# Performance work log

Hardware: AMD Instinct MI355X
Metric: run time of the kernel (lower is better)

## Reference

```python
import jax, jax.numpy as jnp
import numpy as np
import math

B, T, C = 2, 2048, 2048
N_HEAD = 16
N_KV = 4
GROUP = N_HEAD // N_KV
HS = C // N_HEAD
WINDOW = 1024
SINK = 4


def setup_inputs() -> dict:
    key = jax.random.key(0)
    ks = jax.random.split(key, 5)
    s = 1.0 / math.sqrt(C)
    return {
        "x": jax.random.normal(ks[0], (B, T, C), dtype=jnp.float32),
        "Wq": jax.random.normal(ks[1], (C, C), dtype=jnp.float32) * s,
        "Wk": jax.random.normal(ks[2], (N_KV * HS, C), dtype=jnp.float32) * s,
        "Wv": jax.random.normal(ks[3], (N_KV * HS, C), dtype=jnp.float32) * s,
        "Wo": jax.random.normal(ks[4], (C, C), dtype=jnp.float32) * s,
    }


def _sliding_window_sink_mask(t):
    i = jnp.arange(t)[:, None]  # query index
    j = jnp.arange(t)[None, :]  # key index
    causal = j <= i
    band = j >= i - (WINDOW - 1)
    mask = causal & band
    mask = mask | (j < SINK)          # sink columns always visible
    mask = mask & ((i >= SINK) | causal)  # sink rows stay strictly causal
    return mask  # (T, T) bool


def reference(x, Wq, Wk, Wv, Wo):
    b, t, c = x.shape
    q = (x @ Wq.T).reshape(b, t, N_HEAD, HS).transpose(0, 2, 1, 3)
    # group q heads by kv head: (B, n_kv, group, T, hs)
    q = q.reshape(b, N_KV, GROUP, t, HS)
    k = (x @ Wk.T).reshape(b, t, N_KV, HS).transpose(0, 2, 1, 3)  # (B, n_kv, T, hs)
    v = (x @ Wv.T).reshape(b, t, N_KV, HS).transpose(0, 2, 1, 3)
    scale = 1.0 / math.sqrt(HS)
    # scores over full TxT (faithful to original, K/V expansion done via broadcast)
    att = jnp.einsum('bkgqd,bkjd->bkgqj', q, k) * scale
    mask = _sliding_window_sink_mask(t)  # (T, T)
    att = jnp.where(mask[None, None, None, :, :], att, -jnp.inf)
    att = jax.nn.softmax(att, axis=-1)
    y = jnp.einsum('bkgqj,bkjd->bkgqd', att, v)
    y = y.reshape(b, N_HEAD, t, HS).transpose(0, 2, 1, 3).reshape(b, t, c)
    return y @ Wo.T
```

## Files before the change

### kernel.cpp

```cpp
#include <hip/hip_runtime.h>


#define T_SEQ 2048
#define NKV   4
#define HS    128
#define CDIM  2048
#define QKVN  3072
#define WIN   1024
#define SINKN 4
#define PSTR  68

typedef __bf16 bf16x8 __attribute__((ext_vector_type(8)));
typedef float  f32x4  __attribute__((ext_vector_type(4)));

#define MFMA16(A, B, C) __builtin_amdgcn_mfma_f32_16x16x32_bf16(A, B, C, 0, 0, 0)
#define EXP2(x) __builtin_amdgcn_exp2f(x)

__device__ inline unsigned short f2bu(float f) {
  unsigned int u = __float_as_uint(f);
  u += 0x7fffu + ((u >> 16) & 1u);
  return (unsigned short)(u >> 16);
}
__device__ inline unsigned int pkhi(float f0, float f1) {
  return __builtin_amdgcn_perm(__float_as_uint(f1), __float_as_uint(f0),
                               0x07060302u);
}
__device__ inline __bf16 us2b(unsigned short u) {
  union { unsigned short u; __bf16 b; } t; t.u = u; return t.b;
}
__device__ inline f32x4 fzero4() { f32x4 z = {0.f, 0.f, 0.f, 0.f}; return z; }

__device__ __forceinline__ void glds16(const void* g, const void* lds_uniform) {
  typedef __attribute__((address_space(1))) void gv;
  typedef __attribute__((address_space(3))) void lv;
  __builtin_amdgcn_global_load_lds((gv*)(unsigned long long)g,
                                   (lv*)(unsigned int)(unsigned long long)lds_uniform,
                                   16, 0, 0);
}

#define SZ_X  8388608
#define SZ_WQ 4194304
#define SZ_WK 1048576
#define OFF_WQ (SZ_X)
#define OFF_WK (SZ_X + SZ_WQ)
#define OFF_WV (OFF_WK + SZ_WK)
#define OFF_WO (OFF_WV + SZ_WK)
#define SZ_ALL (OFF_WO + SZ_WQ)

__global__ __launch_bounds__(256) void f2b_all(const float* __restrict__ x,
                                               const float* __restrict__ wq,
                                               const float* __restrict__ wk,
                                               const float* __restrict__ wv,
                                               const float* __restrict__ wo,
                                               unsigned short* __restrict__ out,
                                               float qs) {
  int i = (blockIdx.x * 256 + threadIdx.x) * 4;
  const float* src; int off; float sc = 1.0f;
  if (i < OFF_WQ)      { src = x;  off = 0; }
  else if (i < OFF_WK) { src = wq; off = OFF_WQ; sc = qs; }
  else if (i < OFF_WV) { src = wk; off = OFF_WK; }
  else if (i < OFF_WO) { src = wv; off = OFF_WV; }
  else                 { src = wo; off = OFF_WO; }
  float4 v = *reinterpret_cast<const float4*>(src + (i - off));
  ushort4 o;
  o.x = f2bu(v.x * sc); o.y = f2bu(v.y * sc);
  o.z = f2bu(v.z * sc); o.w = f2bu(v.w * sc);
  *reinterpret_cast<ushort4*>(out + i) = o;
}

__device__ inline void storeC(unsigned short* p, float v) { *p = f2bu(v); }
__device__ inline void storeC(float* p, float v) { *p = v; }

template <typename OutT>
__global__ __launch_bounds__(512, 2) void gemm_bn192(const unsigned short* __restrict__ A,
                                                     const unsigned short* __restrict__ B,
                                                     OutT* __restrict__ C,
                                                     int M, int N, int K) {
  __shared__ __align__(16) unsigned short As[2][16384];
  __shared__ __align__(16) unsigned short Bs[2][12288];
  const int tid  = threadIdx.x;
  const int wave = tid >> 6, lane = tid & 63;
  const int quad = lane >> 4, l16 = lane & 15;
  const int wmi  = wave >> 1, wni = wave & 1;
  const int sx   = ((l16 >> 3) & 1) << 5;

  const int tmn  = M >> 8;
  const int qq   = gridDim.x >> 3;
  const int swzb = (blockIdx.x & 7) * qq + (blockIdx.x >> 3);
  const int tm   = (swzb % tmn) << 8;
  const int tn   = (swzb / tmn) * 192;

  const int logl = (lane * 16) ^ (((lane >> 5) & 1) << 5);
  const int srow = logl >> 6;
  const int scol = (logl & 63) >> 1;
  const int NT   = K >> 6;

  auto issueA = [&](int tt, int ch) {
    glds16(&A[(size_t)(tm + (ch & 15) * 16 + srow) * K + (tt << 6) + (ch >> 4) * 32 + scol],
           (const char*)As + ((tt & 1) << 15) + ch * 1024);
  };
  auto issueB = [&](int tt, int kh, int rb) {
    glds16(&B[(size_t)(tn + rb * 16 + srow) * K + (tt << 6) + kh * 32 + scol],
           (const char*)Bs + (tt & 1) * 24576 + (kh * 12 + rb) * 1024);
  };
  const int g3kh = (wave >= 4) ? 1 : 0;
  const int g3rb = (wave >= 4) ? (wave - 4) : (8 + wave);

  f32x4 acc[4][6];
#pragma unroll
  for (int i = 0; i < 4; ++i)
#pragma unroll
    for (int j = 0; j < 6; ++j) acc[i][j] = fzero4();

  issueA(0, wave); issueA(0, 8 + wave); issueB(0, 0, wave);
  issueA(0, 16 + wave); issueA(0, 24 + wave); issueB(0, 1, 4 + wave);
  issueB(0, g3kh, g3rb);
  if (NT > 1) {
    issueA(1, wave); issueA(1, 8 + wave); issueB(1, 0, wave);
    asm volatile("s_waitcnt vmcnt(3)" ::: "memory");
  } else {
    asm volatile("s_waitcnt vmcnt(0)" ::: "memory");
  }
  __builtin_amdgcn_s_barrier();

  for (int t = 0; t < NT; ++t) {
    const char* Asc = (const char*)As + ((t & 1) << 15);
    const char* Bsc = (const char*)Bs + (t & 1) * 24576;
    const bool h1 = (t + 1 < NT), h2 = (t + 2 < NT);
    bf16x8 aq[4], bq[6];

#pragma unroll
    for (int g = 0; g < 6; ++g)
      bq[g] = *reinterpret_cast<const bf16x8*>(
          Bsc + (((wni * 96 + g * 16 + l16) << 6) + ((quad * 16) ^ sx)));
#pragma unroll
    for (int f = 0; f < 4; ++f)
      aq[f] = *reinterpret_cast<const bf16x8*>(
          Asc + (((wmi * 64 + f * 16 + l16) << 6) + ((quad * 16) ^ sx)));
    if (h1) {
      issueA(t + 1, 16 + wave); issueA(t + 1, 24 + wave);
      issueB(t + 1, 1, 4 + wave); issueB(t + 1, g3kh, g3rb);
    }
    __builtin_amdgcn_s_barrier();
    asm volatile("s_waitcnt lgkmcnt(0)" ::: "memory");
    __builtin_amdgcn_s_setprio(1);
#pragma unroll
    for (int f = 0; f < 4; ++f)
#pragma unroll
      for (int g = 0; g < 6; ++g) acc[f][g] = MFMA16(aq[f], bq[g], acc[f][g]);
    __builtin_amdgcn_s_setprio(0);
    if (h1) asm volatile("s_waitcnt vmcnt(7)" ::: "memory");
    else    asm volatile("s_waitcnt vmcnt(0)" ::: "memory");
    __builtin_amdgcn_s_barrier();

#pragma unroll
    for (int g = 0; g < 6; ++g)
      bq[g] = *reinterpret_cast<const bf16x8*>(
          Bsc + (12288 + ((wni * 96 + g * 16 + l16) << 6) + ((quad * 16) ^ sx)));
#pragma unroll
    for (int f = 0; f < 4; ++f)
      aq[f] = *reinterpret_cast<const bf16x8*>(
          Asc + (16384 + ((wmi * 64 + f * 16 + l16) << 6) + ((quad * 16) ^ sx)));
    if (h2) {
      issueA(t + 2, wave); issueA(t + 2, 8 + wave); issueB(t + 2, 0, wave);
    }
    __builtin_amdgcn_s_barrier();
    asm volatile("s_waitcnt lgkmcnt(0)" ::: "memory");
    __builtin_amdgcn_s_setprio(1);
#pragma unroll
    for (int f = 0; f < 4; ++f)
#pragma unroll
      for (int g = 0; g < 6; ++g) acc[f][g] = MFMA16(aq[f], bq[g], acc[f][g]);
    __builtin_amdgcn_s_setprio(0);
    if (h2)      asm volatile("s_waitcnt vmcnt(7)" ::: "memory");
    else if (h1) asm volatile("s_waitcnt vmcnt(4)" ::: "memory");
    else         asm volatile("s_waitcnt vmcnt(0)" ::: "memory");
    __builtin_amdgcn_s_barrier();
  }

#pragma unroll
  for (int fi = 0; fi < 4; ++fi)
#pragma unroll
    for (int g = 0; g < 6; ++g)
#pragma unroll
      for (int r = 0; r < 4; ++r) {
        const int row = tm + wmi * 64 + fi * 16 + quad * 4 + r;
        const int col = tn + wni * 96 + g * 16 + l16;
        storeC(&C[(size_t)row * N + col], acc[fi][g][r]);
      }
}

template <typename OutT>
__global__ __launch_bounds__(512, 2) void gemm_bn128(const unsigned short* __restrict__ A,
                                                     const unsigned short* __restrict__ B,
                                                     OutT* __restrict__ C,
                                                     int M, int N, int K) {
  __shared__ __align__(16) unsigned short As[2][16384];
  __shared__ __align__(16) unsigned short Bs[2][8192];
  const int tid  = threadIdx.x;
  const int wave = tid >> 6, lane = tid & 63;
  const int quad = lane >> 4, l16 = lane & 15;
  const int wmi  = wave >> 1, wni = wave & 1;
  const int sx   = ((l16 >> 3) & 1) << 5;

  const int tmn  = M >> 8;
  const int qq   = gridDim.x >> 3;
  const int swzb = (blockIdx.x & 7) * qq + (blockIdx.x >> 3);
  const int tm   = (swzb % tmn) << 8;
  const int tn   = (swzb / tmn) << 7;

  const int logl = (lane * 16) ^ (((lane >> 5) & 1) << 5);
  const int srow = logl >> 6;
  const int scol = (logl & 63) >> 1;
  const int NT   = K >> 6;

  auto issueA = [&](int tt, int ch) {
    glds16(&A[(size_t)(tm + (ch & 15) * 16 + srow) * K + (tt << 6) + (ch >> 4) * 32 + scol],
           (const char*)As + ((tt & 1) << 15) + ch * 1024);
  };
  auto issueB = [&](int tt, int ch) {
    glds16(&B[(size_t)(tn + (ch & 7) * 16 + srow) * K + (tt << 6) + (ch >> 3) * 32 + scol],
           (const char*)Bs + ((tt & 1) << 14) + ch * 1024);
  };

  f32x4 acc[4][4];
#pragma unroll
  for (int i = 0; i < 4; ++i)
#pragma unroll
    for (int j = 0; j < 4; ++j) acc[i][j] = fzero4();

  issueB(0, wave);     issueA(0, wave);      issueA(0, 8 + wave);
  issueB(0, 8 + wave); issueA(0, 16 + wave); issueA(0, 24 + wave);
  if (NT > 1) {
    issueB(1, wave); issueA(1, wave); issueA(1, 8 + wave);
    asm volatile("s_waitcnt vmcnt(6)" ::: "memory");
  } else {
    asm volatile("s_waitcnt vmcnt(3)" ::: "memory");
  }
  __builtin_amdgcn_s_barrier();

  for (int t = 0; t < NT; ++t) {
    const char* Asc = (const char*)As + ((t & 1) << 15);
    const char* Bsc = (const char*)Bs + ((t & 1) << 14);
    const bool h1 = (t + 1 < NT), h2 = (t + 2 < NT);
    bf16x8 aq[4], bq[4];

#pragma unroll
    for (int g = 0; g < 4; ++g)
      bq[g] = *reinterpret_cast<const bf16x8*>(
          Bsc + (((wni * 64 + g * 16 + l16) << 6) + ((quad * 16) ^ sx)));
#pragma unroll
    for (int f = 0; f < 4; ++f)
      aq[f] = *reinterpret_cast<const bf16x8*>(
          Asc + (((wmi * 64 + f * 16 + l16) << 6) + ((quad * 16) ^ sx)));
    if (h1) {
      issueB(t + 1, 8 + wave); issueA(t + 1, 16 + wave); issueA(t + 1, 24 + wave);
    }
    __builtin_amdgcn_s_barrier();
    asm volatile("s_waitcnt lgkmcnt(0)" ::: "memory");
    __builtin_amdgcn_s_setprio(1);
#pragma unroll
    for (int f = 0; f < 4; ++f)
#pragma unroll
      for (int g = 0; g < 4; ++g) acc[f][g] = MFMA16(aq[f], bq[g], acc[f][g]);
    __builtin_amdgcn_s_setprio(0);
    if (h1) asm volatile("s_waitcnt vmcnt(6)" ::: "memory");
    else    asm volatile("s_waitcnt vmcnt(0)" ::: "memory");
    __builtin_amdgcn_s_barrier();

#pragma unroll
    for (int g = 0; g < 4; ++g)
      bq[g] = *reinterpret_cast<const bf16x8*>(
          Bsc + (8192 + ((wni * 64 + g * 16 + l16) << 6) + ((quad * 16) ^ sx)));
#pragma unroll
    for (int f = 0; f < 4; ++f)
      aq[f] = *reinterpret_cast<const bf16x8*>(
          Asc + (16384 + ((wmi * 64 + f * 16 + l16) << 6) + ((quad * 16) ^ sx)));
    if (h2) {
      issueB(t + 2, wave); issueA(t + 2, wave); issueA(t + 2, 8 + wave);
    }
    __builtin_amdgcn_s_barrier();
    asm volatile("s_waitcnt lgkmcnt(0)" ::: "memory");
    __builtin_amdgcn_s_setprio(1);
#pragma unroll
    for (int f = 0; f < 4; ++f)
#pragma unroll
      for (int g = 0; g < 4; ++g) acc[f][g] = MFMA16(aq[f], bq[g], acc[f][g]);
    __builtin_amdgcn_s_setprio(0);
    if (h2)      asm volatile("s_waitcnt vmcnt(6)" ::: "memory");
    else if (h1) asm volatile("s_waitcnt vmcnt(3)" ::: "memory");
    else         asm volatile("s_waitcnt vmcnt(0)" ::: "memory");
    __builtin_amdgcn_s_barrier();
  }

#pragma unroll
  for (int fi = 0; fi < 4; ++fi)
#pragma unroll
    for (int g = 0; g < 4; ++g)
#pragma unroll
      for (int r = 0; r < 4; ++r) {
        const int row = tm + wmi * 64 + fi * 16 + quad * 4 + r;
        const int col = tn + wni * 64 + g * 16 + l16;
        storeC(&C[(size_t)row * N + col], acc[fi][g][r]);
      }
}

__global__ __launch_bounds__(256) void kvpack(const unsigned short* __restrict__ QKV,
                                              unsigned short* __restrict__ Kp,
                                              unsigned short* __restrict__ Vp) {
  const int tid  = threadIdx.x;
  const int kt64 = blockIdx.x;
  const int bk   = blockIdx.y;
  const int b = bk >> 2, kvh = bk & 3;
  const int kt = kt64 * 64;
  const int bT = b * T_SEQ;
  const int dq = tid & 15;

  unsigned short* kdst = &Kp[(size_t)(bk * 32 + kt64) * 8192];
#pragma unroll
  for (int it = 0; it < 4; ++it) {
    int key = it * 16 + (tid >> 4);
    float4 v = *reinterpret_cast<const float4*>(
        &QKV[(size_t)(bT + kt + key) * QKVN + 2048 + kvh * HS + dq * 8]);
    int c = dq >> 2, quad = dq & 3, nt = key & 3, l16s = key >> 2;
    *reinterpret_cast<float4*>(
        &kdst[((size_t)((c * 4 + nt) * 64 + quad * 16 + l16s)) * 8]) = v;
  }

#pragma unroll
  for (int it = 0; it < 4; ++it) {
    int key = it * 16 + (tid >> 4);
    float4 v = *reinterpret_cast<const float4*>(
        &QKV[(size_t)(bT + kt + key) * QKVN + 2560 + kvh * HS + dq * 8]);
    const unsigned short* pv = reinterpret_cast<const unsigned short*>(&v);
    int kt32 = kt64 * 2 + (key >> 5);
    int quad = (key & 31) >> 3, j = key & 7;
    unsigned short* vdst = &Vp[(size_t)(bk * 64 + kt32) * 4096];
#pragma unroll
    for (int j2 = 0; j2 < 8; ++j2) {
      int d = dq * 8 + j2, dt = d >> 4, l16v = d & 15;
      vdst[((size_t)(dt * 64 + quad * 16 + l16v)) * 8 + j] = pv[j2];
    }
  }
}

__global__ __launch_bounds__(256) void attn_kernel(const unsigned short* __restrict__ QKV,
                                                   const unsigned short* __restrict__ Kp,
                                                   const unsigned short* __restrict__ Vp,
                                                   unsigned short* __restrict__ Y) {
  __shared__ __align__(16) unsigned short KVs[16384];
  __shared__ __align__(16) unsigned short Ps[4 * 32 * PSTR];
  unsigned short* Ks = KVs;
  unsigned short* Vs = KVs + 8192;

  const int tid  = threadIdx.x;
  const int wave = tid >> 6, lane = tid & 63;
  const int quad = lane >> 4, l16 = lane & 15;
  const int qt0 = (int)(gridDim.x - 1 - blockIdx.x) * 32;
  const int kvh = blockIdx.y, b = blockIdx.z;
  const int h   = kvh * 4 + wave;
  const int bk  = b * NKV + kvh;
  const int bT  = b * T_SEQ;
  unsigned short* Pw = &Ps[wave * 32 * PSTR];

  bf16x8 qa[2][4];
#pragma unroll
  for (int mt = 0; mt < 2; ++mt)
#pragma unroll
    for (int c = 0; c < 4; ++c)
      qa[mt][c] = *reinterpret_cast<const bf16x8*>(
          &QKV[(size_t)(bT + qt0 + mt * 16 + l16) * QKVN + h * HS + c * 32 + quad * 8]);

  bf16x8 ones;
#pragma unroll
  for (int j = 0; j < 8; ++j) ones[j] = us2b(0x3F80);

  f32x4 o[2][9];
#pragma unroll
  for (int mt = 0; mt < 2; ++mt)
#pragma unroll
    for (int dt = 0; dt < 9; ++dt) o[mt][dt] = fzero4();

  const int start = (qt0 >= 1024) ? ((qt0 - 1023) & ~63) : 0;
  const int sink  = (start > 0) ? 1 : 0;
  const int nch   = ((qt0 + 32 - start + 63) >> 6) + sink;

  for (int ci = 0; ci < nch; ++ci) {
    const bool is_sink = (sink && ci == 0);
    const int  kt  = is_sink ? 0 : start + (ci - sink) * 64;
    const int  rem = qt0 + 32 - kt;
    const int  kcmax = is_sink ? 1 : (rem >= 64 ? 2 : ((rem + 31) >> 5));
    const bool full  = !is_sink && (kt + 63 <= qt0) && (kt >= qt0 - 992);

    __syncthreads();
    {
      const unsigned short* kg = &Kp[(size_t)(bk * 32 + (kt >> 6)) * 8192 + lane * 8];
      const unsigned short* vg = &Vp[(size_t)(bk * 64 + (kt >> 5)) * 4096 + lane * 8];
#pragma unroll
      for (int i = 0; i < 4; ++i) {
        int part = wave * 4 + i;
        glds16(kg + part * 512, &Ks[part * 512]);
        glds16(vg + part * 512, &Vs[part * 512]);
      }
    }
    __syncthreads();

    f32x4 s[2][4];
#pragma unroll
    for (int nt = 0; nt < 4; ++nt) { s[0][nt] = fzero4(); s[1][nt] = fzero4(); }
#pragma unroll
    for (int c = 0; c < 4; ++c) {
#pragma unroll
      for (int nt = 0; nt < 4; ++nt) {
        bf16x8 kf = *reinterpret_cast<const bf16x8*>(&Ks[(c * 4 + nt) * 512 + lane * 8]);
        s[0][nt] = MFMA16(qa[0][c], kf, s[0][nt]);
        s[1][nt] = MFMA16(qa[1][c], kf, s[1][nt]);
      }
    }

    if (full) {
#pragma unroll
      for (int mt = 0; mt < 2; ++mt)
#pragma unroll
        for (int r = 0; r < 4; ++r) {
          const int row = mt * 16 + quad * 4 + r;
          uint2 pk;
          pk.x = pkhi(EXP2(s[mt][0][r]), EXP2(s[mt][1][r]));
          pk.y = pkhi(EXP2(s[mt][2][r]), EXP2(s[mt][3][r]));
          *reinterpret_cast<uint2*>(&Pw[row * PSTR + l16 * 4]) = pk;
        }
    } else {
#pragma unroll
      for (int mt = 0; mt < 2; ++mt)
#pragma unroll
        for (int r = 0; r < 4; ++r) {
          const int row = mt * 16 + quad * 4 + r;
          const int qi  = qt0 + row;
          float p[4];
#pragma unroll
          for (int nt = 0; nt < 4; ++nt) {
            int kj = kt + l16 * 4 + nt;
            bool ok = ((kj <= qi) && (kj + (WIN - 1) >= qi)) ||
                      ((kj < SINKN) && (qi >= SINKN));
            p[nt] = ok ? EXP2(s[mt][nt][r]) : 0.f;
          }
          uint2 pk;
          pk.x = pkhi(p[0], p[1]);
          pk.y = pkhi(p[2], p[3]);
          *reinterpret_cast<uint2*>(&Pw[row * PSTR + l16 * 4]) = pk;
        }
    }
    asm volatile("s_waitcnt lgkmcnt(0)" ::: "memory");

#pragma unroll
    for (int kc = 0; kc < 2; ++kc)
      if (kc < kcmax) {
#pragma unroll
        for (int mt = 0; mt < 2; ++mt) {
          bf16x8 pf = *reinterpret_cast<const bf16x8*>(
              &Pw[(mt * 16 + l16) * PSTR + kc * 32 + quad * 8]);
#pragma unroll
          for (int dt = 0; dt < 8; ++dt) {
            bf16x8 vf = *reinterpret_cast<const bf16x8*>(
                &Vs[kc * 4096 + dt * 512 + lane * 8]);
            o[mt][dt] = MFMA16(pf, vf, o[mt][dt]);
          }
          o[mt][8] = MFMA16(pf, ones, o[mt][8]);
        }
      }
  }

  __syncthreads();
  unsigned short* Yst = KVs;
#pragma unroll
  for (int mt = 0; mt < 2; ++mt) {
    float inv[4];
#pragma unroll
    for (int r = 0; r < 4; ++r) inv[r] = __builtin_amdgcn_rcpf(o[mt][8][r]);
#pragma unroll
    for (int dt = 0; dt < 8; ++dt)
#pragma unroll
      for (int r = 0; r < 4; ++r)
        Yst[(mt * 16 + quad * 4 + r) * 512 + wave * 128 + dt * 16 + l16] =
            f2bu(o[mt][dt][r] * inv[r]);
  }
  __syncthreads();
#pragma unroll
  for (int it = 0; it < 8; ++it) {
    int idx = it * 256 + tid;
    int row = idx >> 6, col = (idx & 63) * 8;
    *reinterpret_cast<uint4*>(
        &Y[(size_t)(bT + qt0 + row) * CDIM + kvh * 512 + col]) =
        *reinterpret_cast<const uint4*>(&Yst[row * 512 + col]);
  }
}

extern "C" void kernel_launch(void* const* d_in, const int* in_sizes, int n_in,
                              void* d_out, int out_size, void* d_ws, size_t ws_size,
                              hipStream_t stream) {
  const float* x  = (const float*)d_in[0];
  const float* Wq = (const float*)d_in[1];
  const float* Wk = (const float*)d_in[2];
  const float* Wv = (const float*)d_in[3];
  const float* Wo = (const float*)d_in[4];
  float* out = (float*)d_out;

  unsigned short* base = (unsigned short*)d_ws;
  unsigned short* xb   = base;
  unsigned short* wqb  = xb + OFF_WQ;
  unsigned short* wob  = xb + OFF_WO;
  unsigned short* QKVb = xb + SZ_ALL;
  unsigned short* Kpb  = wqb;
  unsigned short* Vpb  = wqb + 2097152;
  unsigned short* Yb   = xb;

  const float qscale = 0.08838834764831845f * 1.4426950408889634f;
  f2b_all<<<SZ_ALL / 1024, 256, 0, stream>>>(x, Wq, Wk, Wv, Wo, xb, qscale);

  gemm_bn192<unsigned short><<<256, 512, 0, stream>>>(xb, wqb, QKVb, 4096, QKVN, 2048);

  kvpack<<<dim3(32, 8), 256, 0, stream>>>(QKVb, Kpb, Vpb);

  attn_kernel<<<dim3(64, 4, 2), 256, 0, stream>>>(QKVb, Kpb, Vpb, Yb);

  gemm_bn128<float><<<256, 512, 0, stream>>>(Yb, wob, out, 4096, 2048, 2048);
}
```

Before: 263.6 us.

## Double-buffer K/V tiles in attention with async prefetch, swizzled P, and reordered grid

The attention kernel now uses two LDS buffers for K and V. It issues the global-to-LDS loads for the next chunk before computing the current one and waits with a partial vmcnt, replacing the two full syncthreads per chunk. The P tile now uses an XOR-swizzled 128-byte row layout instead of padded rows to avoid bank conflicts. MFMA sections get raised wave priority, and the grid is flattened so consecutive blocks cover all batch/kv-head pairs for the same query tile, which aims to balance the uneven causal work. LDS use roughly doubles, which may lower occupancy.

```diff
diff --git a/kernel.cpp b/kernel.cpp
--- a/kernel.cpp
+++ b/kernel.cpp
@@ -8,7 +8,6 @@
 #define QKVN  3072
 #define WIN   1024
 #define SINKN 4
-#define PSTR  68
 
 typedef __bf16 bf16x8 __attribute__((ext_vector_type(8)));
 typedef float  f32x4  __attribute__((ext_vector_type(4)));
@@ -348,20 +347,20 @@
                                                    const unsigned short* __restrict__ Kp,
                                                    const unsigned short* __restrict__ Vp,
                                                    unsigned short* __restrict__ Y) {
-  __shared__ __align__(16) unsigned short KVs[16384];
-  __shared__ __align__(16) unsigned short Ps[4 * 32 * PSTR];
-  unsigned short* Ks = KVs;
-  unsigned short* Vs = KVs + 8192;
+  __shared__ __align__(16) unsigned short Ks[2][8192];
+  __shared__ __align__(16) unsigned short Vs[2][8192];
+  __shared__ __align__(16) unsigned short Ps[4 * 2048];
 
   const int tid  = threadIdx.x;
   const int wave = tid >> 6, lane = tid & 63;
   const int quad = lane >> 4, l16 = lane & 15;
-  const int qt0 = (int)(gridDim.x - 1 - blockIdx.x) * 32;
-  const int kvh = blockIdx.y, b = blockIdx.z;
-  const int h   = kvh * 4 + wave;
-  const int bk  = b * NKV + kvh;
-  const int bT  = b * T_SEQ;
-  unsigned short* Pw = &Ps[wave * 32 * PSTR];
+  const int bk   = blockIdx.x & 7;
+  const int seq  = blockIdx.x >> 3;
+  const int qt0  = (63 - seq) * 32;
+  const int kvh  = bk & 3, b = bk >> 2;
+  const int h    = kvh * 4 + wave;
+  const int bT   = b * T_SEQ;
+  char* Pw = (char*)&Ps[wave * 2048];
 
   bf16x8 qa[2][4];
 #pragma unroll
@@ -385,38 +384,50 @@
   const int sink  = (start > 0) ? 1 : 0;
   const int nch   = ((qt0 + 32 - start + 63) >> 6) + sink;
 
+  auto stage = [&](int ci, int buf) {
+    const int kt = (sink && ci == 0) ? 0 : start + (ci - sink) * 64;
+    const unsigned short* kg = &Kp[(size_t)(bk * 32 + (kt >> 6)) * 8192 + lane * 8];
+    const unsigned short* vg = &Vp[(size_t)(bk * 64 + (kt >> 5)) * 4096 + lane * 8];
+#pragma unroll
+    for (int i = 0; i < 4; ++i) {
+      int part = wave * 4 + i;
+      glds16(kg + part * 512, &Ks[buf][part * 512]);
+      glds16(vg + part * 512, &Vs[buf][part * 512]);
+    }
+  };
+
+  stage(0, 0);
+
   for (int ci = 0; ci < nch; ++ci) {
+    const int  buf = ci & 1;
     const bool is_sink = (sink && ci == 0);
     const int  kt  = is_sink ? 0 : start + (ci - sink) * 64;
     const int  rem = qt0 + 32 - kt;
     const int  kcmax = is_sink ? 1 : (rem >= 64 ? 2 : ((rem + 31) >> 5));
     const bool full  = !is_sink && (kt + 63 <= qt0) && (kt >= qt0 - 992);
 
-    __syncthreads();
-    {
-      const unsigned short* kg = &Kp[(size_t)(bk * 32 + (kt >> 6)) * 8192 + lane * 8];
-      const unsigned short* vg = &Vp[(size_t)(bk * 64 + (kt >> 5)) * 4096 + lane * 8];
-#pragma unroll
-      for (int i = 0; i < 4; ++i) {
-        int part = wave * 4 + i;
-        glds16(kg + part * 512, &Ks[part * 512]);
-        glds16(vg + part * 512, &Vs[part * 512]);
-      }
-    }
-    __syncthreads();
+    if (ci + 1 < nch) {
+      stage(ci + 1, buf ^ 1);
+      asm volatile("s_waitcnt vmcnt(8)" ::: "memory");
+    } else {
+      asm volatile("s_waitcnt vmcnt(0)" ::: "memory");
+    }
+    __builtin_amdgcn_s_barrier();
 
     f32x4 s[2][4];
 #pragma unroll
     for (int nt = 0; nt < 4; ++nt) { s[0][nt] = fzero4(); s[1][nt] = fzero4(); }
+    __builtin_amdgcn_s_setprio(1);
 #pragma unroll
     for (int c = 0; c < 4; ++c) {
 #pragma unroll
       for (int nt = 0; nt < 4; ++nt) {
-        bf16x8 kf = *reinterpret_cast<const bf16x8*>(&Ks[(c * 4 + nt) * 512 + lane * 8]);
+        bf16x8 kf = *reinterpret_cast<const bf16x8*>(&Ks[buf][(c * 4 + nt) * 512 + lane * 8]);
         s[0][nt] = MFMA16(qa[0][c], kf, s[0][nt]);
         s[1][nt] = MFMA16(qa[1][c], kf, s[1][nt]);
       }
     }
+    __builtin_amdgcn_s_setprio(0);
 
     if (full) {
 #pragma unroll
@@ -427,7 +438,8 @@
           uint2 pk;
           pk.x = pkhi(EXP2(s[mt][0][r]), EXP2(s[mt][1][r]));
           pk.y = pkhi(EXP2(s[mt][2][r]), EXP2(s[mt][3][r]));
-          *reinterpret_cast<uint2*>(&Pw[row * PSTR + l16 * 4]) = pk;
+          *reinterpret_cast<uint2*>(
+              Pw + ((row * 128 + l16 * 8) ^ ((row & 7) << 4))) = pk;
         }
     } else {
 #pragma unroll
@@ -447,31 +459,37 @@
           uint2 pk;
           pk.x = pkhi(p[0], p[1]);
           pk.y = pkhi(p[2], p[3]);
-          *reinterpret_cast<uint2*>(&Pw[row * PSTR + l16 * 4]) = pk;
+          *reinterpret_cast<uint2*>(
+              Pw + ((row * 128 + l16 * 8) ^ ((row & 7) << 4))) = pk;
         }
     }
     asm volatile("s_waitcnt lgkmcnt(0)" ::: "memory");
 
+    __builtin_amdgcn_s_setprio(1);
 #pragma unroll
     for (int kc = 0; kc < 2; ++kc)
       if (kc < kcmax) {
 #pragma unroll
         for (int mt = 0; mt < 2; ++mt) {
+          const int prow = mt * 16 + l16;
           bf16x8 pf = *reinterpret_cast<const bf16x8*>(
-              &Pw[(mt * 16 + l16) * PSTR + kc * 32 + quad * 8]);
+              Pw + ((prow * 128 + kc * 64 + quad * 16) ^ ((prow & 7) << 4)));
 #pragma unroll
           for (int dt = 0; dt < 8; ++dt) {
             bf16x8 vf = *reinterpret_cast<const bf16x8*>(
-                &Vs[kc * 4096 + dt * 512 + lane * 8]);
+                &Vs[buf][kc * 4096 + dt * 512 + lane * 8]);
             o[mt][dt] = MFMA16(pf, vf, o[mt][dt]);
           }
           o[mt][8] = MFMA16(pf, ones, o[mt][8]);
         }
       }
+    __builtin_amdgcn_s_setprio(0);
+    asm volatile("" ::: "memory");
+    __builtin_amdgcn_s_barrier();
   }
 
   __syncthreads();
-  unsigned short* Yst = KVs;
+  unsigned short* Yst = &Ks[0][0];
 #pragma unroll
   for (int mt = 0; mt < 2; ++mt) {
     float inv[4];
@@ -521,7 +539,7 @@
 
   kvpack<<<dim3(32, 8), 256, 0, stream>>>(QKVb, Kpb, Vpb);
 
-  attn_kernel<<<dim3(64, 4, 2), 256, 0, stream>>>(QKVb, Kpb, Vpb, Yb);
+  attn_kernel<<<512, 256, 0, stream>>>(QKVb, Kpb, Vpb, Yb);
 
   gemm_bn128<float><<<256, 512, 0, stream>>>(Yb, wob, out, 4096, 2048, 2048);
 }
```

Result: faster. 249.0 us (-5.5%).
